# Optimization experiments

Hardware: AMD Instinct MI355X
Metric: run time of the kernel (lower is better)

Reference implementation:

```python
import jax, jax.numpy as jnp
import numpy as np

DIM = 512
DIM_TIME = 64
DIM_FF = 2048
B, L = 2, 512
EPS = 1e-5


def _layer_norm(x, g, b):
    mu = jnp.mean(x, axis=-1, keepdims=True)
    var = jnp.mean((x - mu) ** 2, axis=-1, keepdims=True)
    return (x - mu) * jax.lax.rsqrt(var + EPS) * g + b


def _sioconv(u, wa, hid_re, hid_im):
    # u: (B, L, Dt) float. Faithful to the FFT/triu construction, expressed as
    # cumulative log-sums (linear conv with all-ones == causal cumsum).
    Bb, Ll, Dt = u.shape
    out = (u @ wa.T).reshape(Bb, Ll, Dt, 2)          # linear_a, view_as_complex
    a_sqr = out[..., 0] ** 2 + out[..., 1] ** 2
    a = (out[..., 0] + 1j * out[..., 1]) * (jax.lax.rsqrt(a_sqr) * jnp.exp(-a_sqr))
    a = jnp.transpose(a, (0, 2, 1))                  # (B, Dt, L)
    a_ln = jnp.log(a)
    S = jnp.cumsum(a_ln, axis=-1)                    # S_k = sum_{j<=k} ln a_j
    S_prev = jnp.concatenate([jnp.zeros_like(S[..., :1]), S[..., :-1]], axis=-1)
    # c[b,d,i,k] = exp(S_k - S_{i-1}) = prod_{j=i..k} a_j, kept for k >= i-1
    diff = S[:, :, None, :] - S_prev[:, :, :, None]  # (B, Dt, L, L)
    idx = jnp.arange(Ll)
    mask = idx[None, :] >= (idx[:, None] - 1)        # k >= i-1 (triu diag=-1)
    c = jnp.where(mask, jnp.exp(diff), 0.0)
    uc = jnp.transpose(u.astype(jnp.complex64), (0, 2, 1))   # (B, Dt, L)
    hidden = (hid_re + 1j * hid_im)[None, :] * jnp.ones((Bb, 1), jnp.complex64)
    xin = jnp.concatenate([hidden[..., None], uc[..., :-1]], axis=-1)  # rolled + h0
    h = jnp.einsum('bdik,bdk->bdi', c, xin)
    h = h.at[:, :, -1].add(uc[:, :, -1])
    return jnp.transpose(h.real, (0, 2, 1)).astype(u.dtype)


def _ffn(x, w1, b1, w2, b2):
    return jax.nn.silu(x @ w1.T + b1) @ w2.T + b2


def setup_inputs() -> dict:
    key = jax.random.key(0)
    ks = jax.random.split(key, 12)
    d, dt, dff = DIM, DIM_TIME, DIM_FF
    return {
        'x': jax.random.normal(ks[0], (B, L, d), jnp.float32),
        'ln1_g': jnp.ones((d,), jnp.float32), 'ln1_b': jnp.zeros((d,), jnp.float32),
        'fc_w': jax.random.normal(ks[1], (dt, d), jnp.float32) * d ** -0.5,
        'fc_b': jnp.zeros((dt,), jnp.float32),
        'lin_in_w': jax.random.normal(ks[2], (dt, d), jnp.float32) * d ** -0.5,
        'lin_in_b': jnp.zeros((dt,), jnp.float32),
        'wa': jax.random.normal(ks[3], (2 * dt, dt), jnp.float32) * dt ** -0.5,
        'hid_re': jax.random.normal(ks[4], (dt,), jnp.float32),
        'hid_im': jax.random.normal(ks[5], (dt,), jnp.float32),
        'lin_out_w': jax.random.normal(ks[6], (d, dt), jnp.float32) * dt ** -0.5,
        'lin_out_b': jnp.zeros((d,), jnp.float32),
        'ln2_g': jnp.ones((d,), jnp.float32), 'ln2_b': jnp.zeros((d,), jnp.float32),
        'w1': jax.random.normal(ks[7], (dff, d), jnp.float32) * d ** -0.5,
        'b1': jnp.zeros((dff,), jnp.float32),
        'w2': jax.random.normal(ks[8], (d, dff), jnp.float32) * dff ** -0.5,
        'b2': jnp.zeros((d,), jnp.float32),
    }


def reference(x, ln1_g, ln1_b, fc_w, fc_b, lin_in_w, lin_in_b, wa, hid_re, hid_im,
              lin_out_w, lin_out_b, ln2_g, ln2_b, w1, b1, w2, b2):
    x_res = x
    xn = _layer_norm(x, ln1_g, ln1_b)
    y = jax.nn.silu(xn @ fc_w.T + fc_b)                  # gate, (B, L, Dt)
    u = xn @ lin_in_w.T + lin_in_b                       # (B, L, Dt)
    h = _sioconv(u, wa, hid_re, hid_im)
    x = (h * y) @ lin_out_w.T + lin_out_b + x_res        # dropout = identity (eval)
    x_res = x
    x = _ffn(_layer_norm(x, ln2_g, ln2_b), w1, b1, w2, b2) + x_res
    return x
```

## Files before the change

### kernel.cpp

```cpp
#include <hip/hip_runtime.h>
#include <math.h>

#define LSEQ 512
#define DMODEL 512
#define DT 64
#define DFF 2048

typedef unsigned short u16;
typedef __attribute__((ext_vector_type(8))) short short8;
typedef __attribute__((ext_vector_type(4))) float f32x4;
typedef __attribute__((ext_vector_type(16))) float f32x16;

__device__ __forceinline__ float wave_sum(float v) {
#pragma unroll
  for (int o = 32; o > 0; o >>= 1) v += __shfl_xor(v, o, 64);
  return v;
}

__device__ __forceinline__ u16 f2bf(float f) {
  unsigned int u = __float_as_uint(f);
  u += 0x7fffu + ((u >> 16) & 1u);
  return (u16)(u >> 16);
}
__device__ __forceinline__ float bf2f(u16 h) {
  return __uint_as_float(((unsigned int)h) << 16);
}
__device__ __forceinline__ void splitbf(float f, u16& h, u16& l) {
  h = f2bf(f);
  l = f2bf(f - bf2f(h));
}


__global__ __launch_bounds__(256) void k_pre(
    const float* __restrict__ w1, const float* __restrict__ w2,
    const float* __restrict__ fcw, const float* __restrict__ liw,
    const float* __restrict__ wa, const float* __restrict__ low,
    const float* __restrict__ x, const float* __restrict__ g1,
    const float* __restrict__ be1,
    u16* __restrict__ w1s, u16* __restrict__ w2s,
    u16* __restrict__ fclh, u16* __restrict__ fcll,
    u16* __restrict__ wah, u16* __restrict__ wal,
    u16* __restrict__ lowh, u16* __restrict__ lowl,
    u16* __restrict__ xnh, u16* __restrict__ xnl)
{
  if (blockIdx.x >= 2152) {
    const int lane = threadIdx.x & 63, wv = threadIdx.x >> 6;
    const int row = (blockIdx.x - 2152) * 4 + wv;
    const float* xr = x + (size_t)row * DMODEL;
    float v[8]; float s = 0.f;
#pragma unroll
    for (int j = 0; j < 8; ++j) { v[j] = xr[lane + 64 * j]; s += v[j]; }
    s = wave_sum(s);
    const float mu = s * (1.f / 512.f);
    float q = 0.f;
#pragma unroll
    for (int j = 0; j < 8; ++j) { float dd = v[j] - mu; q += dd * dd; }
    q = wave_sum(q);
    const float rstd = rsqrtf(q * (1.f / 512.f) + 1e-5f);
#pragma unroll
    for (int j = 0; j < 8; ++j) {
      int idx = lane + 64 * j;
      float o = (v[j] - mu) * rstd * g1[idx] + be1[idx];
      u16 h, l; splitbf(o, h, l);
      xnh[(size_t)row * DMODEL + idx] = h;
      xnl[(size_t)row * DMODEL + idx] = l;
    }
    return;
  }
  int i = blockIdx.x * 256 + threadIdx.x;
  if (i >= 550912) return;
  if (i < 262144) {
    int r = i >> 7, c0 = (i & 127) << 2;
    float4 v = ((const float4*)w1)[i];
    ushort4 o;
    o.x = f2bf(v.x); o.y = f2bf(v.y); o.z = f2bf(v.z); o.w = f2bf(v.w);
    int lane = (r & 31) + (((c0 & 15) >> 3) << 5);
    int flat = (r >> 5) * 16384 + (c0 >> 4) * 512 + lane * 8 + (c0 & 7);
    *(ushort4*)(w1s + flat) = o;
    return;
  }
  if (i < 524288) {
    int ii = i - 262144;
    int r = ii >> 9, c0 = (ii & 511) << 2;
    float4 v = ((const float4*)w2)[ii];
    ushort4 o;
    o.x = f2bf(v.x); o.y = f2bf(v.y); o.z = f2bf(v.z); o.w = f2bf(v.w);
    int lane = (r & 31) + (((c0 & 15) >> 3) << 5);
    int flat = (r >> 5) * 65536 + (c0 >> 4) * 512 + lane * 8 + (c0 & 7);
    *(ushort4*)(w2s + flat) = o;
    return;
  }
  const float* s; int j; u16 *dh, *dl;
  if (i < 532480)      { s = fcw; j = i - 524288;        dh = fclh; dl = fcll; }
  else if (i < 540672) { s = liw; j = i - 532480 + 8192; dh = fclh; dl = fcll; }
  else if (i < 542720) { s = wa;  j = i - 540672;        dh = wah;  dl = wal;  }
  else                 { s = low; j = i - 542720;        dh = lowh; dl = lowl; }
  int soff = (i < 532480) ? i - 524288 :
             (i < 540672) ? i - 532480 :
             (i < 542720) ? i - 540672 : i - 542720;
  float4 v = ((const float4*)s)[soff];
  ushort4 oh, ol;
  splitbf(v.x, oh.x, ol.x); splitbf(v.y, oh.y, ol.y);
  splitbf(v.z, oh.z, ol.z); splitbf(v.w, oh.w, ol.w);
  ((ushort4*)dh)[j] = oh;
  ((ushort4*)dl)[j] = ol;
}

__global__ __launch_bounds__(512) void k_fa(
    const u16* __restrict__ xnh, const u16* __restrict__ xnl,
    const u16* __restrict__ fclh, const u16* __restrict__ fcll,
    const u16* __restrict__ wah, const u16* __restrict__ wal,
    const float* __restrict__ fcb, const float* __restrict__ lib,
    float* __restrict__ y_o, float* __restrict__ u_o,
    float* __restrict__ ar_o, float* __restrict__ ai_o)
{
  __shared__ __align__(16) u16 ush[16][80];
  __shared__ __align__(16) u16 usl[16][80];
  const int w = threadIdx.x >> 6, lane = threadIdx.x & 63;
  const int mt = blockIdx.x;
  const int lr = lane & 15, lk = lane >> 4;

  {
    const size_t aoff = (size_t)(mt * 16 + lr) * DMODEL + lk * 8;
    const size_t boff = (size_t)(w * 16 + lr) * DMODEL + lk * 8;
    f32x4 acc = {};
#pragma unroll 4
    for (int k = 0; k < DMODEL; k += 32) {
      short8 ah = *(const short8*)(xnh + aoff + k);
      short8 al = *(const short8*)(xnl + aoff + k);
      short8 bh = *(const short8*)(fclh + boff + k);
      short8 bl = *(const short8*)(fcll + boff + k);
      acc = __builtin_amdgcn_mfma_f32_16x16x32_bf16(ah, bh, acc, 0, 0, 0);
      acc = __builtin_amdgcn_mfma_f32_16x16x32_bf16(ah, bl, acc, 0, 0, 0);
      acc = __builtin_amdgcn_mfma_f32_16x16x32_bf16(al, bh, acc, 0, 0, 0);
    }
    const int c = w * 16 + lr;
#pragma unroll
    for (int j = 0; j < 4; ++j) {
      int rl = lk * 4 + j;
      int row = mt * 16 + rl;
      float v = acc[j];
      if (c < DT) {
        v += fcb[c];
        y_o[row * DT + c] = v / (1.f + expf(-v));
      } else {
        int d = c - DT;
        v += lib[d];
        u_o[row * DT + d] = v;
        u16 h, l; splitbf(v, h, l);
        ush[rl][d] = h; usl[rl][d] = l;
      }
    }
  }
  __syncthreads();
  {
    const size_t boff = (size_t)(w * 16 + lr) * DT + lk * 8;
    f32x4 acc = {};
#pragma unroll
    for (int ks = 0; ks < 2; ++ks) {
      short8 ah = *(const short8*)&ush[lr][ks * 32 + lk * 8];
      short8 al = *(const short8*)&usl[lr][ks * 32 + lk * 8];
      short8 bh = *(const short8*)(wah + boff + ks * 32);
      short8 bl = *(const short8*)(wal + boff + ks * 32);
      acc = __builtin_amdgcn_mfma_f32_16x16x32_bf16(ah, bh, acc, 0, 0, 0);
      acc = __builtin_amdgcn_mfma_f32_16x16x32_bf16(ah, bl, acc, 0, 0, 0);
      acc = __builtin_amdgcn_mfma_f32_16x16x32_bf16(al, bh, acc, 0, 0, 0);
    }
    const int c = w * 16 + lr;
#pragma unroll
    for (int j = 0; j < 4; ++j) {
      float v = acc[j];
      float p = __shfl_xor(v, 1, 64);
      float re = (lane & 1) ? p : v;
      float im = (lane & 1) ? v : p;
      float asq = re * re + im * im;
      float sc = rsqrtf(asq) * expf(-asq);
      int row = mt * 16 + lk * 4 + j;
      int d = c >> 1;
      if (lane & 1) ai_o[row * DT + d] = im * sc;
      else          ar_o[row * DT + d] = re * sc;
    }
  }
}

__global__ __launch_bounds__(64) void k_scan2(
    const float* __restrict__ u, const float* __restrict__ ar, const float* __restrict__ ai,
    const float* __restrict__ hr, const float* __restrict__ hi, float* __restrict__ h_o)
{
  const int blk = blockIdx.x;
  const int b = blk >> 6, d = blk & 63;
  const int lane = threadIdx.x;
  const size_t base = (size_t)b * LSEQ * DT + d;
  const int i0 = lane * 8;

  float a_r[8], a_i[8], b_r[8], b_i[8];
#pragma unroll
  for (int e = 0; e < 8; ++e) {
    int i = i0 + e;
    a_r[e] = ar[base + (size_t)i * DT];
    a_i[e] = ai[base + (size_t)i * DT];
    if (i >= 2)      { b_r[e] = u[base + (size_t)(i - 2) * DT]; b_i[e] = 0.f; }
    else if (i == 1) { b_r[e] = hr[d]; b_i[e] = hi[d]; }
    else             { b_r[e] = 0.f;   b_i[e] = 0.f; }
  }

  float Ar = 1.f, Ai = 0.f, Br = 0.f, Bi = 0.f;
#pragma unroll
  for (int e = 0; e < 8; ++e) {
    float nBr = fmaf(Ar, b_r[e], fmaf(-Ai, b_i[e], Br));
    float nBi = fmaf(Ar, b_i[e], fmaf( Ai, b_r[e], Bi));
    float nAr = Ar * a_r[e] - Ai * a_i[e];
    float nAi = Ar * a_i[e] + Ai * a_r[e];
    Ar = nAr; Ai = nAi; Br = nBr; Bi = nBi;
  }

#pragma unroll
  for (int dlt = 1; dlt < 64; dlt <<= 1) {
    float Ar2 = __shfl_down(Ar, dlt, 64);
    float Ai2 = __shfl_down(Ai, dlt, 64);
    float Br2 = __shfl_down(Br, dlt, 64);
    float Bi2 = __shfl_down(Bi, dlt, 64);
    if (lane + dlt < 64) {
      float nAr = Ar * Ar2 - Ai * Ai2;
      float nAi = Ar * Ai2 + Ai * Ar2;
      float nBr = fmaf(Ar, Br2, fmaf(-Ai, Bi2, Br));
      float nBi = fmaf(Ar, Bi2, fmaf( Ai, Br2, Bi));
      Ar = nAr; Ai = nAi; Br = nBr; Bi = nBi;
    }
  }

  float A1r = __shfl_down(Ar, 1, 64), A1i = __shfl_down(Ai, 1, 64);
  float B1r = __shfl_down(Br, 1, 64), B1i = __shfl_down(Bi, 1, 64);
  if (lane == 63) { A1r = 1.f; A1i = 0.f; B1r = 0.f; B1i = 0.f; }
  const float r512 = u[base + (size_t)(LSEQ - 2) * DT];
  float rr = fmaf(A1r, r512, B1r);
  float ri = fmaf(A1i, r512, B1i);

  const float uL = u[base + (size_t)(LSEQ - 1) * DT];
#pragma unroll
  for (int e = 7; e >= 0; --e) {
    int i = i0 + e;
    float nr = fmaf(a_r[e], rr, fmaf(-a_i[e], ri, b_r[e]));
    float ni = fmaf(a_r[e], ri, fmaf( a_i[e], rr, b_i[e]));
    rr = nr; ri = ni;
    float outv = rr;
    if (i == LSEQ - 1) outv += uL;
    h_o[base + (size_t)i * DT] = outv;
  }
}

__global__ __launch_bounds__(1024) void k_midln(
    const float* __restrict__ h, const float* __restrict__ y,
    const u16* __restrict__ lowh, const u16* __restrict__ lowl,
    const float* __restrict__ lob, const float* __restrict__ x,
    const float* __restrict__ g2, const float* __restrict__ be2,
    float* __restrict__ x2_o, u16* __restrict__ xn2s)
{
  __shared__ __align__(16) u16 hyh[16][80];
  __shared__ __align__(16) u16 hyl[16][80];
  __shared__ float x2s[16][520];
  const int tid = threadIdx.x;
  const int w = tid >> 6, lane = tid & 63;
  const int lr = lane & 15, lk = lane >> 4;
  const int mt = blockIdx.x;

  {
    int r = tid >> 6, d = tid & 63;
    int row = mt * 16 + r;
    float v = h[row * DT + d] * y[row * DT + d];
    u16 hh, ll; splitbf(v, hh, ll);
    hyh[r][d] = hh; hyl[r][d] = ll;
  }
  __syncthreads();

#pragma unroll
  for (int t = 0; t < 2; ++t) {
    const int nt = w * 2 + t;
    const size_t boff = (size_t)(nt * 16 + lr) * DT + lk * 8;
    f32x4 acc = {};
#pragma unroll
    for (int ks = 0; ks < 2; ++ks) {
      short8 ah = *(const short8*)&hyh[lr][ks * 32 + lk * 8];
      short8 al = *(const short8*)&hyl[lr][ks * 32 + lk * 8];
      short8 bh = *(const short8*)(lowh + boff + ks * 32);
      short8 bl = *(const short8*)(lowl + boff + ks * 32);
      acc = __builtin_amdgcn_mfma_f32_16x16x32_bf16(ah, bh, acc, 0, 0, 0);
      acc = __builtin_amdgcn_mfma_f32_16x16x32_bf16(ah, bl, acc, 0, 0, 0);
      acc = __builtin_amdgcn_mfma_f32_16x16x32_bf16(al, bh, acc, 0, 0, 0);
    }
    const int c = nt * 16 + lr;
#pragma unroll
    for (int j = 0; j < 4; ++j) {
      int rl = lk * 4 + j;
      int row = mt * 16 + rl;
      float v = acc[j] + lob[c] + x[(size_t)row * DMODEL + c];
      x2s[rl][c] = v;
      x2_o[(size_t)row * DMODEL + c] = v;
    }
  }
  __syncthreads();

  {
    const int r = w;
    const int row = mt * 16 + r;
    float v[8]; float s = 0.f;
#pragma unroll
    for (int j = 0; j < 8; ++j) { v[j] = x2s[r][lane + 64 * j]; s += v[j]; }
    s = wave_sum(s);
    const float mu = s * (1.f / 512.f);
    float q = 0.f;
#pragma unroll
    for (int j = 0; j < 8; ++j) { float dd = v[j] - mu; q += dd * dd; }
    q = wave_sum(q);
    const float rstd = rsqrtf(q * (1.f / 512.f) + 1e-5f);
    const int t32 = row >> 5, r32 = row & 31;
#pragma unroll
    for (int j = 0; j < 8; ++j) {
      int idx = lane + 64 * j;
      float o = (v[j] - mu) * rstd * g2[idx] + be2[idx];
      int lane_s = r32 + (((idx & 15) >> 3) << 5);
      xn2s[t32 * 16384 + (idx >> 4) * 512 + lane_s * 8 + (idx & 7)] = f2bf(o);
    }
  }
}

__global__ __launch_bounds__(256) void k_ffn1(
    const u16* __restrict__ As, const u16* __restrict__ Bs,
    const float* __restrict__ bias, u16* __restrict__ Cs)
{
  const int w = threadIdx.x >> 6, lane = threadIdx.x & 63;
  const int mt = blockIdx.x, nt = blockIdx.y * 4 + w;
  const u16* a = As + mt * 16384 + lane * 8;
  const u16* b = Bs + nt * 16384 + lane * 8;
  f32x16 acc = {};
#pragma unroll 8
  for (int kb = 0; kb < 32; ++kb)
    acc = __builtin_amdgcn_mfma_f32_32x32x16_bf16(*(const short8*)(a + kb * 512),
                                                  *(const short8*)(b + kb * 512),
                                                  acc, 0, 0, 0);
  const int l31 = lane & 31, hi = lane >> 5;
  const int col = nt * 32 + l31;
  const float bb = bias[col];
  const int kb_c = col >> 4;
  const int half_c = (col & 15) >> 3, e_c = col & 7;
#pragma unroll
  for (int r = 0; r < 16; ++r) {
    int row32 = (r & 3) + 8 * (r >> 2) + 4 * hi;
    float v = acc[r] + bb;
    v = v / (1.f + expf(-v));
    int lane_s = row32 + (half_c << 5);
    Cs[mt * 65536 + kb_c * 512 + lane_s * 8 + e_c] = f2bf(v);
  }
}

__global__ __launch_bounds__(256) void k_ffn2(
    const u16* __restrict__ As, const u16* __restrict__ Bs,
    const float* __restrict__ b2, const float* __restrict__ x2,
    float* __restrict__ out)
{
  __shared__ float red[4][16][64];
  const int w = threadIdx.x >> 6, lane = threadIdx.x & 63;
  const int mt = blockIdx.x, nt = blockIdx.y;
  const u16* a = As + mt * 65536 + w * 32 * 512 + lane * 8;
  const u16* b = Bs + nt * 65536 + w * 32 * 512 + lane * 8;
  f32x16 acc = {};
#pragma unroll 8
  for (int kb = 0; kb < 32; ++kb)
    acc = __builtin_amdgcn_mfma_f32_32x32x16_bf16(*(const short8*)(a + kb * 512),
                                                  *(const short8*)(b + kb * 512),
                                                  acc, 0, 0, 0);
#pragma unroll
  for (int r = 0; r < 16; ++r) red[w][r][lane] = acc[r];
  __syncthreads();
  for (int s = threadIdx.x; s < 1024; s += 256) {
    int r = s >> 6, l = s & 63;
    float v = red[0][r][l] + red[1][r][l] + red[2][r][l] + red[3][r][l];
    int row = mt * 32 + (r & 3) + 8 * (r >> 2) + 4 * (l >> 5);
    int col = nt * 32 + (l & 31);
    out[(size_t)row * DMODEL + col] =
        v + b2[col] + x2[(size_t)row * DMODEL + col];
  }
}

extern "C" void kernel_launch(void* const* d_in, const int* in_sizes, int n_in,
                              void* d_out, int out_size, void* d_ws, size_t ws_size,
                              hipStream_t stream) {
  const float* x    = (const float*)d_in[0];
  const float* ln1g = (const float*)d_in[1];
  const float* ln1b = (const float*)d_in[2];
  const float* fcw  = (const float*)d_in[3];
  const float* fcb  = (const float*)d_in[4];
  const float* liw  = (const float*)d_in[5];
  const float* lib  = (const float*)d_in[6];
  const float* wa   = (const float*)d_in[7];
  const float* hidr = (const float*)d_in[8];
  const float* hidi = (const float*)d_in[9];
  const float* low  = (const float*)d_in[10];
  const float* lob  = (const float*)d_in[11];
  const float* ln2g = (const float*)d_in[12];
  const float* ln2b = (const float*)d_in[13];
  const float* w1   = (const float*)d_in[14];
  const float* b1   = (const float*)d_in[15];
  const float* w2   = (const float*)d_in[16];
  const float* b2   = (const float*)d_in[17];
  float* out = (float*)d_out;
  float* ws  = (float*)d_ws;

  float* y_   = ws;
  float* u_   = y_  + 65536;
  float* ar_  = u_  + 65536;
  float* ai_  = ar_ + 65536;
  float* h_   = ai_ + 65536;
  float* x2_  = h_  + 65536;
  u16* p = (u16*)(x2_ + 524288);
  u16* xnh  = p;            p += 524288;
  u16* xnl  = p;            p += 524288;
  u16* xn2s = p;            p += 524288;
  u16* h1s  = p;            p += 2097152;
  u16* w1s  = p;            p += 1048576;
  u16* w2s  = p;            p += 1048576;
  u16* fclh = p;            p += 65536;
  u16* fcll = p;            p += 65536;
  u16* wah  = p;            p += 8192;
  u16* wal  = p;            p += 8192;
  u16* lowh = p;            p += 32768;
  u16* lowl = p;            p += 32768;

  k_pre<<<2408, 256, 0, stream>>>(w1, w2, fcw, liw, wa, low, x, ln1g, ln1b,
                                  w1s, w2s, fclh, fcll, wah, wal, lowh, lowl,
                                  xnh, xnl);
  k_fa<<<64, 512, 0, stream>>>(xnh, xnl, fclh, fcll, wah, wal, fcb, lib,
                               y_, u_, ar_, ai_);
  k_scan2<<<128, 64, 0, stream>>>(u_, ar_, ai_, hidr, hidi, h_);
  k_midln<<<64, 1024, 0, stream>>>(h_, y_, lowh, lowl, lob, x, ln2g, ln2b,
                                   x2_, xn2s);
  k_ffn1<<<dim3(32, 16), 256, 0, stream>>>(xn2s, w1s, b1, h1s);
  k_ffn2<<<dim3(32, 16), 256, 0, stream>>>(h1s, w2s, b2, x2_, out);
}
```

Measured before the change: 62.86 us.

## Fuse LayerNorm1 and weight prep into k_fa, split small weights on the fly

Removes the separate k_pre kernel. LayerNorm1 is now computed per block directly into shared memory. The w1/w2 bf16 conversion runs in 256 extra blocks of k_fa that execute alongside the 64 compute blocks. The small weights (fc, lin_in, wa, lin_out) are now read as fp32 and split into hi/lo bf16 inside the MFMA loops instead of being pre-split into global buffers. This saves one launch and the xn/weight round-trips, at the cost of redundant split arithmetic per block and competition between the prep blocks and the compute blocks.

```diff
diff --git a/kernel.cpp b/kernel.cpp
--- a/kernel.cpp
+++ b/kernel.cpp
@@ -29,23 +29,67 @@
   h = f2bf(f);
   l = f2bf(f - bf2f(h));
 }
-
-
-__global__ __launch_bounds__(256) void k_pre(
-    const float* __restrict__ w1, const float* __restrict__ w2,
-    const float* __restrict__ fcw, const float* __restrict__ liw,
-    const float* __restrict__ wa, const float* __restrict__ low,
+__device__ __forceinline__ void split8(const float* __restrict__ p,
+                                       short8& bh, short8& bl) {
+  float4 a = *(const float4*)p;
+  float4 b = *(const float4*)(p + 4);
+  float vv[8] = {a.x, a.y, a.z, a.w, b.x, b.y, b.z, b.w};
+#pragma unroll
+  for (int e = 0; e < 8; ++e) {
+    u16 h, l; splitbf(vv[e], h, l);
+    bh[e] = (short)h; bl[e] = (short)l;
+  }
+}
+
+
+__global__ __launch_bounds__(512) void k_fa(
     const float* __restrict__ x, const float* __restrict__ g1,
     const float* __restrict__ be1,
-    u16* __restrict__ w1s, u16* __restrict__ w2s,
-    u16* __restrict__ fclh, u16* __restrict__ fcll,
-    u16* __restrict__ wah, u16* __restrict__ wal,
-    u16* __restrict__ lowh, u16* __restrict__ lowl,
-    u16* __restrict__ xnh, u16* __restrict__ xnl)
+    const float* __restrict__ fcw, const float* __restrict__ liw,
+    const float* __restrict__ wa,
+    const float* __restrict__ fcb, const float* __restrict__ lib,
+    const float* __restrict__ w1, const float* __restrict__ w2,
+    float* __restrict__ y_o, float* __restrict__ u_o,
+    float* __restrict__ ar_o, float* __restrict__ ai_o,
+    u16* __restrict__ w1s, u16* __restrict__ w2s)
 {
-  if (blockIdx.x >= 2152) {
-    const int lane = threadIdx.x & 63, wv = threadIdx.x >> 6;
-    const int row = (blockIdx.x - 2152) * 4 + wv;
+  const int blk = blockIdx.x;
+  if (blk >= 64) {
+    for (int i = (blk - 64) * 512 + threadIdx.x; i < 524288; i += 131072) {
+      if (i < 262144) {
+        int r = i >> 7, c0 = (i & 127) << 2;
+        float4 v = ((const float4*)w1)[i];
+        ushort4 o;
+        o.x = f2bf(v.x); o.y = f2bf(v.y); o.z = f2bf(v.z); o.w = f2bf(v.w);
+        int lane_s = (r & 31) + (((c0 & 15) >> 3) << 5);
+        int flat = (r >> 5) * 16384 + (c0 >> 4) * 512 + lane_s * 8 + (c0 & 7);
+        *(ushort4*)(w1s + flat) = o;
+      } else {
+        int ii = i - 262144;
+        int r = ii >> 9, c0 = (ii & 511) << 2;
+        float4 v = ((const float4*)w2)[ii];
+        ushort4 o;
+        o.x = f2bf(v.x); o.y = f2bf(v.y); o.z = f2bf(v.z); o.w = f2bf(v.w);
+        int lane_s = (r & 31) + (((c0 & 15) >> 3) << 5);
+        int flat = (r >> 5) * 65536 + (c0 >> 4) * 512 + lane_s * 8 + (c0 & 7);
+        *(ushort4*)(w2s + flat) = o;
+      }
+    }
+    return;
+  }
+  __shared__ __align__(16) u16 xsh[16][520];
+  __shared__ __align__(16) u16 xsl[16][520];
+  __shared__ __align__(16) u16 ush[16][80];
+  __shared__ __align__(16) u16 usl[16][80];
+  const int tid = threadIdx.x;
+  const int wv = tid >> 6, lane = tid & 63;
+  const int lr = lane & 15, lk = lane >> 4;
+  const int mt = blk;
+
+#pragma unroll
+  for (int rr = 0; rr < 2; ++rr) {
+    const int r = wv * 2 + rr;
+    const int row = mt * 16 + r;
     const float* xr = x + (size_t)row * DMODEL;
     float v[8]; float s = 0.f;
 #pragma unroll
@@ -62,79 +106,27 @@
       int idx = lane + 64 * j;
       float o = (v[j] - mu) * rstd * g1[idx] + be1[idx];
       u16 h, l; splitbf(o, h, l);
-      xnh[(size_t)row * DMODEL + idx] = h;
-      xnl[(size_t)row * DMODEL + idx] = l;
-    }
-    return;
-  }
-  int i = blockIdx.x * 256 + threadIdx.x;
-  if (i >= 550912) return;
-  if (i < 262144) {
-    int r = i >> 7, c0 = (i & 127) << 2;
-    float4 v = ((const float4*)w1)[i];
-    ushort4 o;
-    o.x = f2bf(v.x); o.y = f2bf(v.y); o.z = f2bf(v.z); o.w = f2bf(v.w);
-    int lane = (r & 31) + (((c0 & 15) >> 3) << 5);
-    int flat = (r >> 5) * 16384 + (c0 >> 4) * 512 + lane * 8 + (c0 & 7);
-    *(ushort4*)(w1s + flat) = o;
-    return;
-  }
-  if (i < 524288) {
-    int ii = i - 262144;
-    int r = ii >> 9, c0 = (ii & 511) << 2;
-    float4 v = ((const float4*)w2)[ii];
-    ushort4 o;
-    o.x = f2bf(v.x); o.y = f2bf(v.y); o.z = f2bf(v.z); o.w = f2bf(v.w);
-    int lane = (r & 31) + (((c0 & 15) >> 3) << 5);
-    int flat = (r >> 5) * 65536 + (c0 >> 4) * 512 + lane * 8 + (c0 & 7);
-    *(ushort4*)(w2s + flat) = o;
-    return;
-  }
-  const float* s; int j; u16 *dh, *dl;
-  if (i < 532480)      { s = fcw; j = i - 524288;        dh = fclh; dl = fcll; }
-  else if (i < 540672) { s = liw; j = i - 532480 + 8192; dh = fclh; dl = fcll; }
-  else if (i < 542720) { s = wa;  j = i - 540672;        dh = wah;  dl = wal;  }
-  else                 { s = low; j = i - 542720;        dh = lowh; dl = lowl; }
-  int soff = (i < 532480) ? i - 524288 :
-             (i < 540672) ? i - 532480 :
-             (i < 542720) ? i - 540672 : i - 542720;
-  float4 v = ((const float4*)s)[soff];
-  ushort4 oh, ol;
-  splitbf(v.x, oh.x, ol.x); splitbf(v.y, oh.y, ol.y);
-  splitbf(v.z, oh.z, ol.z); splitbf(v.w, oh.w, ol.w);
-  ((ushort4*)dh)[j] = oh;
-  ((ushort4*)dl)[j] = ol;
-}
-
-__global__ __launch_bounds__(512) void k_fa(
-    const u16* __restrict__ xnh, const u16* __restrict__ xnl,
-    const u16* __restrict__ fclh, const u16* __restrict__ fcll,
-    const u16* __restrict__ wah, const u16* __restrict__ wal,
-    const float* __restrict__ fcb, const float* __restrict__ lib,
-    float* __restrict__ y_o, float* __restrict__ u_o,
-    float* __restrict__ ar_o, float* __restrict__ ai_o)
-{
-  __shared__ __align__(16) u16 ush[16][80];
-  __shared__ __align__(16) u16 usl[16][80];
-  const int w = threadIdx.x >> 6, lane = threadIdx.x & 63;
-  const int mt = blockIdx.x;
-  const int lr = lane & 15, lk = lane >> 4;
-
+      xsh[r][idx] = h;
+      xsl[r][idx] = l;
+    }
+  }
+  __syncthreads();
+
+  const int c = wv * 16 + lr;
   {
-    const size_t aoff = (size_t)(mt * 16 + lr) * DMODEL + lk * 8;
-    const size_t boff = (size_t)(w * 16 + lr) * DMODEL + lk * 8;
+    const float* brow = (c < DT) ? (fcw + (size_t)c * DMODEL)
+                                 : (liw + (size_t)(c - DT) * DMODEL);
     f32x4 acc = {};
 #pragma unroll 4
     for (int k = 0; k < DMODEL; k += 32) {
-      short8 ah = *(const short8*)(xnh + aoff + k);
-      short8 al = *(const short8*)(xnl + aoff + k);
-      short8 bh = *(const short8*)(fclh + boff + k);
-      short8 bl = *(const short8*)(fcll + boff + k);
+      short8 ah = *(const short8*)&xsh[lr][k + lk * 8];
+      short8 al = *(const short8*)&xsl[lr][k + lk * 8];
+      short8 bh, bl;
+      split8(brow + k + lk * 8, bh, bl);
       acc = __builtin_amdgcn_mfma_f32_16x16x32_bf16(ah, bh, acc, 0, 0, 0);
       acc = __builtin_amdgcn_mfma_f32_16x16x32_bf16(ah, bl, acc, 0, 0, 0);
       acc = __builtin_amdgcn_mfma_f32_16x16x32_bf16(al, bh, acc, 0, 0, 0);
     }
-    const int c = w * 16 + lr;
 #pragma unroll
     for (int j = 0; j < 4; ++j) {
       int rl = lk * 4 + j;
@@ -154,19 +146,18 @@
   }
   __syncthreads();
   {
-    const size_t boff = (size_t)(w * 16 + lr) * DT + lk * 8;
+    const float* warow = wa + (size_t)c * DT;
     f32x4 acc = {};
 #pragma unroll
     for (int ks = 0; ks < 2; ++ks) {
       short8 ah = *(const short8*)&ush[lr][ks * 32 + lk * 8];
       short8 al = *(const short8*)&usl[lr][ks * 32 + lk * 8];
-      short8 bh = *(const short8*)(wah + boff + ks * 32);
-      short8 bl = *(const short8*)(wal + boff + ks * 32);
+      short8 bh, bl;
+      split8(warow + ks * 32 + lk * 8, bh, bl);
       acc = __builtin_amdgcn_mfma_f32_16x16x32_bf16(ah, bh, acc, 0, 0, 0);
       acc = __builtin_amdgcn_mfma_f32_16x16x32_bf16(ah, bl, acc, 0, 0, 0);
       acc = __builtin_amdgcn_mfma_f32_16x16x32_bf16(al, bh, acc, 0, 0, 0);
     }
-    const int c = w * 16 + lr;
 #pragma unroll
     for (int j = 0; j < 4; ++j) {
       float v = acc[j];
@@ -251,9 +242,9 @@
 
 __global__ __launch_bounds__(1024) void k_midln(
     const float* __restrict__ h, const float* __restrict__ y,
-    const u16* __restrict__ lowh, const u16* __restrict__ lowl,
-    const float* __restrict__ lob, const float* __restrict__ x,
-    const float* __restrict__ g2, const float* __restrict__ be2,
+    const float* __restrict__ low, const float* __restrict__ lob,
+    const float* __restrict__ x, const float* __restrict__ g2,
+    const float* __restrict__ be2,
     float* __restrict__ x2_o, u16* __restrict__ xn2s)
 {
   __shared__ __align__(16) u16 hyh[16][80];
@@ -276,14 +267,14 @@
 #pragma unroll
   for (int t = 0; t < 2; ++t) {
     const int nt = w * 2 + t;
-    const size_t boff = (size_t)(nt * 16 + lr) * DT + lk * 8;
+    const float* brow = low + (size_t)(nt * 16 + lr) * DT;
     f32x4 acc = {};
 #pragma unroll
     for (int ks = 0; ks < 2; ++ks) {
       short8 ah = *(const short8*)&hyh[lr][ks * 32 + lk * 8];
       short8 al = *(const short8*)&hyl[lr][ks * 32 + lk * 8];
-      short8 bh = *(const short8*)(lowh + boff + ks * 32);
-      short8 bl = *(const short8*)(lowl + boff + ks * 32);
+      short8 bh, bl;
+      split8(brow + ks * 32 + lk * 8, bh, bl);
       acc = __builtin_amdgcn_mfma_f32_16x16x32_bf16(ah, bh, acc, 0, 0, 0);
       acc = __builtin_amdgcn_mfma_f32_16x16x32_bf16(ah, bl, acc, 0, 0, 0);
       acc = __builtin_amdgcn_mfma_f32_16x16x32_bf16(al, bh, acc, 0, 0, 0);
@@ -413,27 +404,15 @@
   float* h_   = ai_ + 65536;
   float* x2_  = h_  + 65536;
   u16* p = (u16*)(x2_ + 524288);
-  u16* xnh  = p;            p += 524288;
-  u16* xnl  = p;            p += 524288;
   u16* xn2s = p;            p += 524288;
   u16* h1s  = p;            p += 2097152;
   u16* w1s  = p;            p += 1048576;
   u16* w2s  = p;            p += 1048576;
-  u16* fclh = p;            p += 65536;
-  u16* fcll = p;            p += 65536;
-  u16* wah  = p;            p += 8192;
-  u16* wal  = p;            p += 8192;
-  u16* lowh = p;            p += 32768;
-  u16* lowl = p;            p += 32768;
-
-  k_pre<<<2408, 256, 0, stream>>>(w1, w2, fcw, liw, wa, low, x, ln1g, ln1b,
-                                  w1s, w2s, fclh, fcll, wah, wal, lowh, lowl,
-                                  xnh, xnl);
-  k_fa<<<64, 512, 0, stream>>>(xnh, xnl, fclh, fcll, wah, wal, fcb, lib,
-                               y_, u_, ar_, ai_);
+
+  k_fa<<<320, 512, 0, stream>>>(x, ln1g, ln1b, fcw, liw, wa, fcb, lib, w1, w2,
+                                y_, u_, ar_, ai_, w1s, w2s);
   k_scan2<<<128, 64, 0, stream>>>(u_, ar_, ai_, hidr, hidi, h_);
-  k_midln<<<64, 1024, 0, stream>>>(h_, y_, lowh, lowl, lob, x, ln2g, ln2b,
-                                   x2_, xn2s);
+  k_midln<<<64, 1024, 0, stream>>>(h_, y_, low, lob, x, ln2g, ln2b, x2_, xn2s);
   k_ffn1<<<dim3(32, 16), 256, 0, stream>>>(xn2s, w1s, b1, h1s);
   k_ffn2<<<dim3(32, 16), 256, 0, stream>>>(h1s, w2s, b2, x2_, out);
 }
```

Result: faster. 53.72 us (-14.5%).
